# Performance work log

Hardware: AMD Instinct MI355X
Metric: run time of the kernel (lower is better)

The kernel has to match this reference:

```python
import jax, jax.numpy as jnp
import numpy as np

B, S, D = 4, 4096, 2048      # batch, seq, model_dim
E = 128                      # emb_dim (hardcoded in module)
H = 128                      # head_dim
TAU = 0.4                    # self.T
BASE = 3.0                   # self.base (gumbel-sigmoid offset)
LN_EPS = 1e-5


def setup_inputs() -> dict:
    key = jax.random.key(0)
    k_x, k_wr, k_wd, k_g = jax.random.split(key, 4)
    x = jax.random.normal(k_x, (B, S, D), dtype=jnp.float32)
    # torch nn.Linear stores weight as [out_features, in_features]
    W_router = jax.random.normal(k_wr, (E, D), dtype=jnp.float32) / np.sqrt(D)
    W_decoder = jax.random.normal(k_wd, (H, E), dtype=jnp.float32) / np.sqrt(E)
    ln_gamma = jnp.ones((E,), dtype=jnp.float32)
    ln_beta = jnp.zeros((E,), dtype=jnp.float32)
    rnn_state = jnp.zeros((E,), dtype=jnp.float32)  # registered buffer, zeros
    # torch: gumbels = -Exp(1).log()  -> standard Gumbel(0,1) noise
    u = jax.random.uniform(k_g, (B, S, H), dtype=jnp.float32, minval=1e-20, maxval=1.0)
    gumbel_noise = -jnp.log(-jnp.log(u))
    return {
        "x": x, "W_router": W_router, "W_decoder": W_decoder,
        "ln_gamma": ln_gamma, "ln_beta": ln_beta, "rnn_state": rnn_state,
        "gumbel_noise": gumbel_noise, "top_k": 32,
    }


def reference(x, W_router, W_decoder, ln_gamma, ln_beta, rnn_state, gumbel_noise, top_k):
    # router linear (no bias): [B,S,D] @ [D,E] -> [B,S,E]
    out = jnp.einsum("bsd,ed->bse", x, W_router)
    full_emb = rnn_state + out
    # LayerNorm over emb dim (biased variance, as torch LayerNorm)
    mu = full_emb.mean(-1, keepdims=True)
    var = full_emb.var(-1, keepdims=True)
    h = (full_emb - mu) / jnp.sqrt(var + LN_EPS) * ln_gamma + ln_beta
    # decoder linear after exact GELU: [B,S,E] @ [E,H] -> [B,S,H]
    logits = jnp.einsum("bse,he->bsh", jax.nn.gelu(h, approximate=False), W_decoder)
    # gumbel-sigmoid (soft): sigmoid((logits + gumbel + offset)/tau)
    binary_approx = jax.nn.sigmoid((logits + gumbel_noise + BASE) / TAU)
    # hard_sample: straight-through round
    binary = jax.lax.stop_gradient(jnp.round(binary_approx) - binary_approx) + binary_approx
    # top-k mask over head_dim
    _, topk_idx = jax.lax.top_k(binary_approx, top_k)            # [B,S,top_k]
    topk_mask = jax.nn.one_hot(topk_idx, H, dtype=binary_approx.dtype).sum(-2)  # [B,S,H]
    cnt = binary.sum(-1, keepdims=True)
    binary = jnp.where(cnt > top_k, topk_mask, binary)
    # fallback: if a token selects nothing, pick argmax of soft scores
    zero_mask = binary.sum(-1, keepdims=True) == 0
    fallback = jax.nn.one_hot(jnp.argmax(binary_approx, axis=-1), H, dtype=binary_approx.dtype)
    binary = jnp.where(zero_mask, fallback, binary)
    binary = binary.reshape(B, S, -1, H)  # [B,S,1,H]
    return binary, binary_approx
```

## Files before the change

kernel.cpp:

```cpp
#include <hip/hip_runtime.h>
#include <math.h>

#define NTOK   16384
#define DDIM   2048
#define EDIM   128
#define HDIM   128
#define TOKT   64
#define NRND   16
#define KRND   128

typedef __attribute__((ext_vector_type(8)))  _Float16 half8;
typedef __attribute__((ext_vector_type(4)))  float    f32x4;
typedef __attribute__((ext_vector_type(16))) float    f32x16;

#define MFMA32 __builtin_amdgcn_mfma_f32_32x32x16_f16

__device__ __forceinline__ int swz(int t, int e) {
  return t * EDIM + ((e & 96) | ((e ^ t) & 31));
}

__device__ __forceinline__ void cvt8(const float4& a, const float4& b,
                                     half8& h, half8& l) {
#pragma unroll
  for (int m = 0; m < 4; ++m) {
    const float v = (&a.x)[m];
    const _Float16 hv = (_Float16)v;
    h[m] = hv; l[m] = (_Float16)((v - (float)hv) * 2048.0f);
  }
#pragma unroll
  for (int m = 0; m < 4; ++m) {
    const float v = (&b.x)[m];
    const _Float16 hv = (_Float16)v;
    h[m + 4] = hv; l[m + 4] = (_Float16)((v - (float)hv) * 2048.0f);
  }
}

__global__ __launch_bounds__(256)
void conv_w(const float* __restrict__ Wr,
            _Float16* __restrict__ wh, _Float16* __restrict__ wl) {
  const int idx  = (int)blockIdx.x * 256 + (int)threadIdx.x;
  const int lane = idx & 63;
  const int ks   = (idx >> 6) & 127;
  const int nt   = idx >> 13;
  const int n    = nt * 32 + (lane & 31);
  const int k0   = ks * 16 + (lane >> 5) * 8;
  half8 h, l;
#pragma unroll
  for (int j = 0; j < 8; ++j) {
    const float w = Wr[(size_t)n * DDIM + k0 + j] * 32.0f;
    const _Float16 hh = (_Float16)w;
    h[j] = hh;
    l[j] = (_Float16)((w - (float)hh) * 2048.0f);
  }
  *(half8*)(wh + (size_t)idx * 8) = h;
  *(half8*)(wl + (size_t)idx * 8) = l;
}

__global__ __launch_bounds__(512, 2)
void fused_router(const float* __restrict__ x,
                  const _Float16* __restrict__ wsh,
                  const _Float16* __restrict__ wsl,
                  const float* __restrict__ Wd,
                  const float* __restrict__ gamma,
                  const float* __restrict__ beta,
                  const float* __restrict__ rnn,
                  const float* __restrict__ gum,
                  float* __restrict__ outb,
                  float* __restrict__ outa) {
  __shared__ char smraw[65536];
  char* const sm = smraw;
  float* const A  = (float*)smraw;
  float* const G4 = (float*)(smraw + 32768);

  const int tid  = (int)threadIdx.x;
  const int wv   = __builtin_amdgcn_readfirstlane(tid >> 6);
  const int lane = tid & 63;
  const int t0   = (int)blockIdx.x * TOKT;

  const int mt = wv >> 2;
  const int nt = wv & 3;

  const int s_tok = (tid & 7) + ((tid >> 6) << 3);
  const int s_s   = (tid >> 3) & 7;
  const int s_row = s_tok & 31;
  const int s_mt  = s_tok >> 5;
  const float* xg = x + (size_t)(t0 + s_tok) * DDIM + s_s * 16;
  const int wbase = (s_s * 2 + s_mt) * 2048;
  const int widx0 = (((0 * 32 + s_row) ^ s_s) * 16);
  const int widx1 = (((1 * 32 + s_row) ^ s_s) * 16);

  const size_t wbf = (size_t)nt * 65536 + (size_t)lane * 8;

  f32x16 hh, cr;
#pragma unroll
  for (int g = 0; g < 16; ++g) { hh[g] = 0.0f; cr[g] = 0.0f; }

  {
    const float4 a0 = *(const float4*)(xg + 0);
    const float4 a1 = *(const float4*)(xg + 4);
    const float4 a2 = *(const float4*)(xg + 8);
    const float4 a3 = *(const float4*)(xg + 12);
    half8 h0, l0, h1, l1;
    cvt8(a0, a1, h0, l0);
    cvt8(a2, a3, h1, l1);
    char* dst = sm;
    *(half8*)(dst + wbase + widx0)        = h0;
    *(half8*)(dst + wbase + 1024 + widx0) = l0;
    *(half8*)(dst + wbase + widx1)        = h1;
    *(half8*)(dst + wbase + 1024 + widx1) = l1;
  }

  for (int r = 0; r < NRND; ++r) {
    __syncthreads();
    float4 p0, p1, p2, p3;
    if (r + 1 < NRND) {
      const float* xn = xg + (r + 1) * KRND;
      p0 = *(const float4*)(xn + 0);
      p1 = *(const float4*)(xn + 4);
      p2 = *(const float4*)(xn + 8);
      p3 = *(const float4*)(xn + 12);
    }
    const char* bb = sm + (r & 1) * 32768;
#pragma unroll
    for (int s = 0; s < 8; ++s) {
      const int fb = (s * 2 + mt) * 2048;
      const int ai = (lane ^ s) * 16;
      const half8 ah = *(const half8*)(bb + fb + ai);
      const half8 al = *(const half8*)(bb + fb + 1024 + ai);
      const size_t wo = wbf + (size_t)(r * 8 + s) * 512;
      const half8 bh = *(const half8*)(wsh + wo);
      const half8 bl = *(const half8*)(wsl + wo);
      hh = MFMA32(ah, bh, hh, 0, 0, 0);
      cr = MFMA32(ah, bl, cr, 0, 0, 0);
      cr = MFMA32(al, bh, cr, 0, 0, 0);
    }
    if (r + 1 < NRND) {
      half8 h0, l0, h1, l1;
      cvt8(p0, p1, h0, l0);
      cvt8(p2, p3, h1, l1);
      char* dst = sm + ((r + 1) & 1) * 32768;
      *(half8*)(dst + wbase + widx0)        = h0;
      *(half8*)(dst + wbase + 1024 + widx0) = l0;
      *(half8*)(dst + wbase + widx1)        = h1;
      *(half8*)(dst + wbase + 1024 + widx1) = l1;
    }
  }
  __syncthreads();

  {
    const int e = nt * 32 + (lane & 31);
    const float rv = rnn[e];
#pragma unroll
    for (int g = 0; g < 16; ++g) {
      const int row = (g & 3) + 8 * (g >> 2) + 4 * (lane >> 5);
      A[swz(mt * 32 + row, e)] =
          hh[g] * (1.0f / 32.0f) + cr[g] * (1.0f / 65536.0f) + rv;
    }
  }
  __syncthreads();

  {
    const float gm0 = gamma[lane], gm1 = gamma[lane + 64];
    const float bt0 = beta[lane],  bt1 = beta[lane + 64];
    for (int tt = wv * 8; tt < wv * 8 + 8; ++tt) {
      const float v0 = A[swz(tt, lane)];
      const float v1 = A[swz(tt, lane + 64)];
      float s = v0 + v1;
#pragma unroll
      for (int m = 32; m; m >>= 1) s += __shfl_xor(s, m);
      const float mu = s * (1.0f / 128.0f);
      const float d0 = v0 - mu, d1 = v1 - mu;
      float q = d0 * d0 + d1 * d1;
#pragma unroll
      for (int m = 32; m; m >>= 1) q += __shfl_xor(q, m);
      const float rstd = 1.0f / sqrtf(q * (1.0f / 128.0f) + 1e-5f);
      const float h0v = d0 * rstd * gm0 + bt0;
      const float h1v = d1 * rstd * gm1 + bt1;
      const float g0 = 0.5f * h0v * (1.0f + erff(h0v * 0.70710678118654752f));
      const float g1 = 0.5f * h1v * (1.0f + erff(h1v * 0.70710678118654752f));
      const int e0a = lane, e1a = lane + 64;
      G4[(tt * 32 + (((e0a >> 2) ^ (tt & 31)))) * 4 + (e0a & 3)] = g0;
      G4[(tt * 32 + (((e1a >> 2) ^ (tt & 31)))) * 4 + (e1a & 3)] = g1;
    }
  }
  __syncthreads();

  {
    const int rbase = wv * 16;
    float acc2[16];
#pragma unroll
    for (int j = 0; j < 16; ++j) acc2[j] = 0.0f;
    const float4* wd4 = (const float4*)(Wd + (size_t)rbase * EDIM);
#pragma unroll 2
    for (int kg = 0; kg < EDIM / 4; ++kg) {
      const float4 gv = *(const float4*)&G4[(lane * 32 + (kg ^ (lane & 31))) * 4];
#pragma unroll
      for (int j = 0; j < 16; ++j) {
        const float4 w = wd4[(size_t)j * (EDIM / 4) + kg];
        acc2[j] = fmaf(gv.x, w.x,
                  fmaf(gv.y, w.y,
                  fmaf(gv.z, w.z,
                  fmaf(gv.w, w.w, acc2[j]))));
      }
    }
    __syncthreads();
#pragma unroll
    for (int j = 0; j < 16; ++j) A[swz(lane, rbase + j)] = acc2[j];
  }
  __syncthreads();

  for (int tt = wv * 8; tt < wv * 8 + 8; ++tt) {
    const size_t T = (size_t)(t0 + tt);
    const float l0 = A[swz(tt, lane)];
    const float l1 = A[swz(tt, lane + 64)];
    const float gn0 = gum[T * HDIM + lane];
    const float gn1 = gum[T * HDIM + lane + 64];
    const float z0 = (l0 + gn0 + 3.0f) * 2.5f;
    const float z1 = (l1 + gn1 + 3.0f) * 2.5f;
    const float ba0 = 1.0f / (1.0f + expf(-z0));
    const float ba1 = 1.0f / (1.0f + expf(-z1));
    const unsigned ub0 = __float_as_uint(ba0);
    const unsigned ub1 = __float_as_uint(ba1);
    const int r0 = ba0 > 0.5f;
    const int r1 = ba1 > 0.5f;
    const int cnt = __popcll(__ballot(r0)) + __popcll(__ballot(r1));
    float bin0, bin1;
    if (cnt > 32) {
      unsigned v = 0u;
#pragma unroll
      for (int b = 29; b >= 0; --b) {
        const unsigned cand = v | (1u << b);
        const int cc = __popcll(__ballot(ub0 >= cand)) + __popcll(__ballot(ub1 >= cand));
        if (cc >= 32) v = cand;
      }
      const int cgt = __popcll(__ballot(ub0 > v)) + __popcll(__ballot(ub1 > v));
      const int r = 32 - cgt;
      const unsigned long long t0b = __ballot(ub0 == v);
      const unsigned long long t1b = __ballot(ub1 == v);
      const int n0 = __popcll(t0b);
      const unsigned long long mlt = (1ull << lane) - 1ull;
      const int rk0 = __popcll(t0b & mlt);
      const int rk1 = n0 + __popcll(t1b & mlt);
      bin0 = (ub0 > v || (ub0 == v && rk0 < r)) ? 1.0f : 0.0f;
      bin1 = (ub1 > v || (ub1 == v && rk1 < r)) ? 1.0f : 0.0f;
    } else if (cnt == 0) {
      float m = fmaxf(ba0, ba1);
#pragma unroll
      for (int mm = 32; mm; mm >>= 1) m = fmaxf(m, __shfl_xor(m, mm));
      const unsigned long long e0b = __ballot(ba0 == m);
      const unsigned long long e1b = __ballot(ba1 == m);
      const int hstar = e0b ? (__ffsll((unsigned long long)e0b) - 1)
                            : (64 + __ffsll((unsigned long long)e1b) - 1);
      bin0 = (lane == hstar) ? 1.0f : 0.0f;
      bin1 = (lane + 64 == hstar) ? 1.0f : 0.0f;
    } else {
      bin0 = r0 ? 1.0f : 0.0f;
      bin1 = r1 ? 1.0f : 0.0f;
    }
    outb[T * HDIM + lane]      = bin0;
    outb[T * HDIM + lane + 64] = bin1;
    outa[T * HDIM + lane]      = ba0;
    outa[T * HDIM + lane + 64] = ba1;
  }
}

extern "C" void kernel_launch(void* const* d_in, const int* in_sizes, int n_in,
                              void* d_out, int out_size, void* d_ws, size_t ws_size,
                              hipStream_t stream) {
  (void)in_sizes; (void)n_in; (void)ws_size; (void)out_size;
  const float* x   = (const float*)d_in[0];
  const float* Wr  = (const float*)d_in[1];
  const float* Wd  = (const float*)d_in[2];
  const float* gm  = (const float*)d_in[3];
  const float* bt  = (const float*)d_in[4];
  const float* rnn = (const float*)d_in[5];
  const float* gum = (const float*)d_in[6];
  float* outb = (float*)d_out;
  float* outa = outb + (size_t)NTOK * HDIM;

  _Float16* wh = (_Float16*)d_ws;
  _Float16* wl = wh + (size_t)EDIM * DDIM;

  conv_w<<<dim3(128), dim3(256), 0, stream>>>(Wr, wh, wl);
  fused_router<<<dim3(NTOK / TOKT), dim3(512), 0, stream>>>(
      x, wh, wl, Wd, gm, bt, rnn, gum, outb, outa);
}
```

Baseline: 280.6 us.

## Split K across two wave groups with 1024-thread blocks and shorten top-k search

Doubles the block to 16 waves, so each pair of wave groups takes half of every K round in the router GEMM, and merges the two partial accumulators through shared memory. The staging loads, LayerNorm, decoder and output loops are re-divided so each wave handles fewer tokens. The top-k bit search now starts from the 0.5 exponent pattern, which is valid because only values above 0.5 are counted, so it runs 24 steps instead of 30. The intent is more waves in flight to hide global loads. The cost is an extra reduction pass with a barrier and tighter register limits under launch_bounds(1024,4).

```diff
diff --git a/kernel.cpp b/kernel.cpp
--- a/kernel.cpp
+++ b/kernel.cpp
@@ -10,7 +10,6 @@
 #define KRND   128
 
 typedef __attribute__((ext_vector_type(8)))  _Float16 half8;
-typedef __attribute__((ext_vector_type(4)))  float    f32x4;
 typedef __attribute__((ext_vector_type(16))) float    f32x16;
 
 #define MFMA32 __builtin_amdgcn_mfma_f32_32x32x16_f16
@@ -56,7 +55,7 @@
   *(half8*)(wl + (size_t)idx * 8) = l;
 }
 
-__global__ __launch_bounds__(512, 2)
+__global__ __launch_bounds__(1024, 4)
 void fused_router(const float* __restrict__ x,
                   const _Float16* __restrict__ wsh,
                   const _Float16* __restrict__ wsl,
@@ -77,17 +76,18 @@
   const int lane = tid & 63;
   const int t0   = (int)blockIdx.x * TOKT;
 
-  const int mt = wv >> 2;
-  const int nt = wv & 3;
-
-  const int s_tok = (tid & 7) + ((tid >> 6) << 3);
-  const int s_s   = (tid >> 3) & 7;
-  const int s_row = s_tok & 31;
-  const int s_mt  = s_tok >> 5;
-  const float* xg = x + (size_t)(t0 + s_tok) * DDIM + s_s * 16;
-  const int wbase = (s_s * 2 + s_mt) * 2048;
-  const int widx0 = (((0 * 32 + s_row) ^ s_s) * 16);
-  const int widx1 = (((1 * 32 + s_row) ^ s_s) * 16);
+  const int kw  = wv >> 3;
+  const int mt  = (wv >> 2) & 1;
+  const int nt  = wv & 3;
+  const int kw4 = kw * 4;
+
+  const int s_tok = (tid & 3) + ((tid >> 6) << 2);
+  const int s_kq  = (tid >> 2) & 15;
+  const int s_s   = s_kq >> 1;
+  const int s_ko  = s_kq & 1;
+  const float* xg = x + (size_t)(t0 + s_tok) * DDIM + s_kq * 8;
+  const int wbase = (s_s * 2 + (s_tok >> 5)) * 2048;
+  const int wslot = ((s_ko * 32 + (s_tok & 31)) ^ s_s ^ (s_ko * 4)) * 16;
 
   const size_t wbf = (size_t)nt * 65536 + (size_t)lane * 8;
 
@@ -98,33 +98,26 @@
   {
     const float4 a0 = *(const float4*)(xg + 0);
     const float4 a1 = *(const float4*)(xg + 4);
-    const float4 a2 = *(const float4*)(xg + 8);
-    const float4 a3 = *(const float4*)(xg + 12);
-    half8 h0, l0, h1, l1;
-    cvt8(a0, a1, h0, l0);
-    cvt8(a2, a3, h1, l1);
-    char* dst = sm;
-    *(half8*)(dst + wbase + widx0)        = h0;
-    *(half8*)(dst + wbase + 1024 + widx0) = l0;
-    *(half8*)(dst + wbase + widx1)        = h1;
-    *(half8*)(dst + wbase + 1024 + widx1) = l1;
+    half8 h, l;
+    cvt8(a0, a1, h, l);
+    *(half8*)(sm + wbase + wslot)        = h;
+    *(half8*)(sm + wbase + 1024 + wslot) = l;
   }
 
   for (int r = 0; r < NRND; ++r) {
     __syncthreads();
-    float4 p0, p1, p2, p3;
+    float4 p0, p1;
     if (r + 1 < NRND) {
       const float* xn = xg + (r + 1) * KRND;
       p0 = *(const float4*)(xn + 0);
       p1 = *(const float4*)(xn + 4);
-      p2 = *(const float4*)(xn + 8);
-      p3 = *(const float4*)(xn + 12);
     }
     const char* bb = sm + (r & 1) * 32768;
 #pragma unroll
-    for (int s = 0; s < 8; ++s) {
+    for (int i = 0; i < 4; ++i) {
+      const int s  = kw4 + i;
       const int fb = (s * 2 + mt) * 2048;
-      const int ai = (lane ^ s) * 16;
+      const int ai = ((lane ^ s ^ ((lane >> 5) << 2)) << 4);
       const half8 ah = *(const half8*)(bb + fb + ai);
       const half8 al = *(const half8*)(bb + fb + 1024 + ai);
       const size_t wo = wbf + (size_t)(r * 8 + s) * 512;
@@ -135,34 +128,41 @@
       cr = MFMA32(al, bh, cr, 0, 0, 0);
     }
     if (r + 1 < NRND) {
-      half8 h0, l0, h1, l1;
-      cvt8(p0, p1, h0, l0);
-      cvt8(p2, p3, h1, l1);
+      half8 h, l;
+      cvt8(p0, p1, h, l);
       char* dst = sm + ((r + 1) & 1) * 32768;
-      *(half8*)(dst + wbase + widx0)        = h0;
-      *(half8*)(dst + wbase + 1024 + widx0) = l0;
-      *(half8*)(dst + wbase + widx1)        = h1;
-      *(half8*)(dst + wbase + 1024 + widx1) = l1;
-    }
-  }
-  __syncthreads();
-
-  {
-    const int e = nt * 32 + (lane & 31);
-    const float rv = rnn[e];
+      *(half8*)(dst + wbase + wslot)        = h;
+      *(half8*)(dst + wbase + 1024 + wslot) = l;
+    }
+  }
+  __syncthreads();
+
+  const int e = nt * 32 + (lane & 31);
+  if (kw == 0) {
 #pragma unroll
     for (int g = 0; g < 16; ++g) {
       const int row = (g & 3) + 8 * (g >> 2) + 4 * (lane >> 5);
       A[swz(mt * 32 + row, e)] =
+          hh[g] * (1.0f / 32.0f) + cr[g] * (1.0f / 65536.0f);
+    }
+  }
+  __syncthreads();
+  if (kw == 1) {
+    const float rv = rnn[e];
+#pragma unroll
+    for (int g = 0; g < 16; ++g) {
+      const int row = (g & 3) + 8 * (g >> 2) + 4 * (lane >> 5);
+      A[swz(mt * 32 + row, e)] +=
           hh[g] * (1.0f / 32.0f) + cr[g] * (1.0f / 65536.0f) + rv;
     }
   }
   __syncthreads();
 
+  const int e0 = wv * 8;
   {
     const float gm0 = gamma[lane], gm1 = gamma[lane + 64];
     const float bt0 = beta[lane],  bt1 = beta[lane + 64];
-    for (int tt = wv * 8; tt < wv * 8 + 8; ++tt) {
+    for (int tt = wv * 4; tt < wv * 4 + 4; ++tt) {
       const float v0 = A[swz(tt, lane)];
       const float v1 = A[swz(tt, lane + 64)];
       float s = v0 + v1;
@@ -186,16 +186,15 @@
   __syncthreads();
 
   {
-    const int rbase = wv * 16;
-    float acc2[16];
-#pragma unroll
-    for (int j = 0; j < 16; ++j) acc2[j] = 0.0f;
-    const float4* wd4 = (const float4*)(Wd + (size_t)rbase * EDIM);
+    float acc2[8];
+#pragma unroll
+    for (int j = 0; j < 8; ++j) acc2[j] = 0.0f;
+    const float4* wd4 = (const float4*)(Wd + (size_t)e0 * EDIM);
 #pragma unroll 2
     for (int kg = 0; kg < EDIM / 4; ++kg) {
       const float4 gv = *(const float4*)&G4[(lane * 32 + (kg ^ (lane & 31))) * 4];
 #pragma unroll
-      for (int j = 0; j < 16; ++j) {
+      for (int j = 0; j < 8; ++j) {
         const float4 w = wd4[(size_t)j * (EDIM / 4) + kg];
         acc2[j] = fmaf(gv.x, w.x,
                   fmaf(gv.y, w.y,
@@ -205,11 +204,11 @@
     }
     __syncthreads();
 #pragma unroll
-    for (int j = 0; j < 16; ++j) A[swz(lane, rbase + j)] = acc2[j];
-  }
-  __syncthreads();
-
-  for (int tt = wv * 8; tt < wv * 8 + 8; ++tt) {
+    for (int j = 0; j < 8; ++j) A[swz(lane, e0 + j)] = acc2[j];
+  }
+  __syncthreads();
+
+  for (int tt = wv * 4; tt < wv * 4 + 4; ++tt) {
     const size_t T = (size_t)(t0 + tt);
     const float l0 = A[swz(tt, lane)];
     const float l1 = A[swz(tt, lane + 64)];
@@ -226,9 +225,9 @@
     const int cnt = __popcll(__ballot(r0)) + __popcll(__ballot(r1));
     float bin0, bin1;
     if (cnt > 32) {
-      unsigned v = 0u;
-#pragma unroll
-      for (int b = 29; b >= 0; --b) {
+      unsigned v = 0x3F000000u;
+#pragma unroll
+      for (int b = 23; b >= 0; --b) {
         const unsigned cand = v | (1u << b);
         const int cc = __popcll(__ballot(ub0 >= cand)) + __popcll(__ballot(ub1 >= cand));
         if (cc >= 32) v = cand;
@@ -282,6 +281,6 @@
   _Float16* wl = wh + (size_t)EDIM * DDIM;
 
   conv_w<<<dim3(128), dim3(256), 0, stream>>>(Wr, wh, wl);
-  fused_router<<<dim3(NTOK / TOKT), dim3(512), 0, stream>>>(
+  fused_router<<<dim3(NTOK / TOKT), dim3(1024), 0, stream>>>(
       x, wh, wl, Wd, gm, bt, rnn, gum, outb, outa);
 }
```

New measurement: 256.1 us. 1.1x faster.
